# Kernel optimization log

Hardware: AMD Instinct MI355X
Metric: run time of the kernel (lower is better)

The kernel has to match this reference:

```python
import jax, jax.numpy as jnp
import numpy as np

E = 1024   # embd_size
H = 16     # head_count
HS = E // H
B = 8
T = 1024   # seq len == input_size
EPS = 1e-5

def _ln(x, g, b):
    m = jnp.mean(x, axis=-1, keepdims=True)
    v = jnp.mean((x - m) ** 2, axis=-1, keepdims=True)
    return (x - m) * jax.lax.rsqrt(v + EPS) * g + b

def setup_inputs() -> dict:
    key = jax.random.key(0)
    ks = jax.random.split(key, 12)
    s_attn = 1.0 / np.sqrt(E)
    s_ff1 = 1.0 / np.sqrt(E)
    s_ff2 = 1.0 / np.sqrt(4 * E)
    return {
        "x": jax.random.normal(ks[0], (B, T, E), dtype=jnp.float32),
        "wq": jax.random.normal(ks[1], (H, E, HS), dtype=jnp.float32) * s_attn,
        "wk": jax.random.normal(ks[2], (H, E, HS), dtype=jnp.float32) * s_attn,
        "wv": jax.random.normal(ks[3], (H, E, HS), dtype=jnp.float32) * s_attn,
        "w_proj": jax.random.normal(ks[4], (E, E), dtype=jnp.float32) * s_attn,
        "b_proj": jnp.zeros((E,), dtype=jnp.float32),
        "w1": jax.random.normal(ks[5], (E, 4 * E), dtype=jnp.float32) * s_ff1,
        "b1": jnp.zeros((4 * E,), dtype=jnp.float32),
        "w2": jax.random.normal(ks[6], (4 * E, E), dtype=jnp.float32) * s_ff2,
        "b2": jnp.zeros((E,), dtype=jnp.float32),
        "g1": jnp.ones((E,), dtype=jnp.float32),
        "be1": jnp.zeros((E,), dtype=jnp.float32),
        "g2": jnp.ones((E,), dtype=jnp.float32),
        "be2": jnp.zeros((E,), dtype=jnp.float32),
    }

def reference(x, wq, wk, wv, w_proj, b_proj, w1, b1, w2, b2, g1, be1, g2, be2):
    Tn = x.shape[1]
    h = _ln(x, g1, be1)
    # per-head projections, batched over heads: [B,T,E] x [H,E,S] -> [B,H,T,S]
    q = jnp.einsum('bte,hes->bhts', h, wq)
    k = jnp.einsum('bte,hes->bhts', h, wk)
    v = jnp.einsum('bte,hes->bhts', h, wv)
    scores = jnp.einsum('bhts,bhus->bhtu', q, k)
    # NOTE: source multiplies by sqrt(T) (x.shape[2] of scores), not 1/sqrt(head_size)
    scores = scores * jnp.float32(Tn) ** 0.5
    causal = jnp.tril(jnp.ones((Tn, Tn), dtype=bool))
    scores = jnp.where(causal, scores, -jnp.inf)
    attn = jax.nn.softmax(scores, axis=-1)
    out = jnp.einsum('bhtu,bhus->bhts', attn, v)           # [B,H,T,S]
    out = out.transpose(0, 2, 1, 3).reshape(x.shape[0], Tn, E)  # concat heads
    out = out @ w_proj + b_proj
    x = x + out
    f = _ln(x, g2, be2)
    f = jax.nn.relu(f @ w1 + b1) @ w2 + b2
    return x + f
```

## Files before the change

### kernel.cpp

```cpp
#include <hip/hip_runtime.h>


typedef unsigned short u16;
typedef __attribute__((ext_vector_type(8))) short  bfx8;
typedef __attribute__((ext_vector_type(4))) float  f32x4;
typedef __attribute__((ext_vector_type(4))) unsigned short u16v4;

#define MFMA16 __builtin_amdgcn_mfma_f32_16x16x32_bf16

__device__ __forceinline__ u16 f2bf(float f) {
    union { float f; unsigned u; } c; c.f = f;
    unsigned r = c.u + 0x7fffu + ((c.u >> 16) & 1u);
    return (u16)(r >> 16);
}
__device__ __forceinline__ float bf2f(u16 b) {
    union { unsigned u; float f; } c; c.u = ((unsigned)b) << 16; return c.f;
}

__device__ __forceinline__ void gl_lds16(const void* g, void* l) {
    void* gg = (void*)g;
    __builtin_amdgcn_global_load_lds(
        (__attribute__((address_space(1))) void*)gg,
        (__attribute__((address_space(3))) void*)l,
        16, 0, 0);
}

__global__ __launch_bounds__(256)
void transpose_split(const float* __restrict__ src, u16* __restrict__ dhi,
                     u16* __restrict__ dlo, int C, int OS,
                     size_t inBS, size_t outBS)
{
    __shared__ float t[64][65];
    const int tid = threadIdx.x;
    const float* s = src + (size_t)blockIdx.z * inBS
                   + ((size_t)blockIdx.y * 64) * C + (size_t)blockIdx.x * 64;
    const size_t obase = (size_t)blockIdx.z * outBS
                       + ((size_t)blockIdx.x * 64) * OS + (size_t)blockIdx.y * 64;
    {
        const int r = tid >> 2, c4 = (tid & 3) * 16;
#pragma unroll
        for (int k = 0; k < 4; ++k) {
            float4 f = *(const float4*)(s + (size_t)r * C + c4 + k * 4);
            t[r][c4 + k*4 + 0] = f.x; t[r][c4 + k*4 + 1] = f.y;
            t[r][c4 + k*4 + 2] = f.z; t[r][c4 + k*4 + 3] = f.w;
        }
    }
    __syncthreads();
    {
        const int c = tid >> 2, r4 = (tid & 3) * 16;
        bfx8 h0, h1, l0, l1;
#pragma unroll
        for (int k = 0; k < 8; ++k) {
            float v0 = t[r4 + k][c];
            float v1 = t[r4 + 8 + k][c];
            u16 a = f2bf(v0), b = f2bf(v1);
            h0[k] = (short)a; h1[k] = (short)b;
            l0[k] = (short)f2bf(v0 - bf2f(a));
            l1[k] = (short)f2bf(v1 - bf2f(b));
        }
        u16* d = dhi + obase + (size_t)c * OS + r4;
        *(bfx8*)d = h0; *(bfx8*)(d + 8) = h1;
        if (dlo) {
            u16* d2 = dlo + obase + (size_t)c * OS + r4;
            *(bfx8*)d2 = l0; *(bfx8*)(d2 + 8) = l1;
        }
    }
}

__global__ __launch_bounds__(256)
void transpose_v(const u16* __restrict__ v, u16* __restrict__ vT)
{
    const int ut = blockIdx.x, h = blockIdx.y, b = blockIdx.z;
    __shared__ u16 t[64][72];
    const int tid = threadIdx.x;
    {
        const int u = tid >> 2, s4 = (tid & 3) * 16;
        const u16* src = v + ((size_t)(b * 1024 + ut * 64 + u)) * 1024 + h * 64 + s4;
        bfx8 a = *(const bfx8*)src;
        bfx8 c = *(const bfx8*)(src + 8);
#pragma unroll
        for (int k = 0; k < 8; ++k) { t[u][s4 + k] = (u16)a[k]; t[u][s4 + 8 + k] = (u16)c[k]; }
    }
    __syncthreads();
    {
        const int s = tid >> 2, u4 = (tid & 3) * 16;
        bfx8 o0, o1;
#pragma unroll
        for (int k = 0; k < 8; ++k) { o0[k] = (short)t[u4 + k][s]; o1[k] = (short)t[u4 + 8 + k][s]; }
        u16* dst = vT + ((size_t)((b * 16 + h) * 64 + s)) * 1024 + ut * 64 + u4;
        *(bfx8*)dst = o0; *(bfx8*)(dst + 8) = o1;
    }
}

__global__ __launch_bounds__(256)
void ln_split(const float* __restrict__ x, const float* __restrict__ g,
              const float* __restrict__ be, u16* __restrict__ hhi,
              u16* __restrict__ hlo)
{
    const int row = blockIdx.x;
    const int tid = threadIdx.x;
    const float4 v = ((const float4*)(x + (size_t)row * 1024))[tid];
    float s  = v.x + v.y + v.z + v.w;
    float s2 = v.x*v.x + v.y*v.y + v.z*v.z + v.w*v.w;
#pragma unroll
    for (int m = 32; m >= 1; m >>= 1) {
        s  += __shfl_xor(s,  m, 64);
        s2 += __shfl_xor(s2, m, 64);
    }
    __shared__ float rs[4], rq[4];
    if ((tid & 63) == 0) { rs[tid >> 6] = s; rq[tid >> 6] = s2; }
    __syncthreads();
    s  = rs[0] + rs[1] + rs[2] + rs[3];
    s2 = rq[0] + rq[1] + rq[2] + rq[3];
    const float mean = s * (1.0f / 1024.0f);
    const float var  = s2 * (1.0f / 1024.0f) - mean * mean;
    const float inv  = rsqrtf(var + 1e-5f);
    const int col0 = tid * 4;
    float hv[4];
    hv[0] = (v.x - mean) * inv * g[col0+0] + be[col0+0];
    hv[1] = (v.y - mean) * inv * g[col0+1] + be[col0+1];
    hv[2] = (v.z - mean) * inv * g[col0+2] + be[col0+2];
    hv[3] = (v.w - mean) * inv * g[col0+3] + be[col0+3];
    u16v4 hb, lb;
#pragma unroll
    for (int k = 0; k < 4; ++k) {
        u16 a = f2bf(hv[k]);
        hb[k] = a;
        lb[k] = f2bf(hv[k] - bf2f(a));
    }
    *(u16v4*)(hhi + (size_t)row * 1024 + col0) = hb;
    if (hlo) *(u16v4*)(hlo + (size_t)row * 1024 + col0) = lb;
}

#define BM 128
#define BN 128
#define BKT 32

template<int FLAGS>
__global__ __launch_bounds__(256, 2)
void gemm_bt(const u16* __restrict__ A, const u16* __restrict__ Bt,
             void* __restrict__ Cout, const float* __restrict__ bias,
             const float* __restrict__ res, int M, int N, int K)
{
    __shared__ u16 As[BM * BKT];
    __shared__ u16 Bs[BN * BKT];
    const int tid  = threadIdx.x;
    const int lane = tid & 63, wave = tid >> 6;
    const int wr = wave >> 1, wc = wave & 1;
    const int li = lane & 15, lg = lane >> 4;
    const size_t m0 = (size_t)blockIdx.y * BM;
    const size_t n0 = (size_t)blockIdx.x * BN;
    f32x4 acc[4][4] = {};

    const int slot0 = tid, slot1 = tid + 256;
    const int r0 = slot0 >> 2, kc0 = (slot0 & 3) * 8;
    const int r1 = slot1 >> 2, kc1 = (slot1 & 3) * 8;

    for (int kt = 0; kt < K; kt += BKT) {
        __syncthreads();
        gl_lds16(A  + (m0 + r0) * K + kt + kc0, As + slot0 * 8);
        gl_lds16(Bt + (n0 + r0) * K + kt + kc0, Bs + slot0 * 8);
        gl_lds16(A  + (m0 + r1) * K + kt + kc1, As + slot1 * 8);
        gl_lds16(Bt + (n0 + r1) * K + kt + kc1, Bs + slot1 * 8);
        __syncthreads();
        bfx8 af[4], bfr[4];
#pragma unroll
        for (int i = 0; i < 4; ++i)
            af[i] = *(const bfx8*)&As[(wr * 64 + i * 16 + li) * BKT + lg * 8];
#pragma unroll
        for (int j = 0; j < 4; ++j)
            bfr[j] = *(const bfx8*)&Bs[(wc * 64 + j * 16 + li) * BKT + lg * 8];
#pragma unroll
        for (int i = 0; i < 4; ++i)
#pragma unroll
            for (int j = 0; j < 4; ++j)
                acc[i][j] = MFMA16(af[i], bfr[j], acc[i][j], 0, 0, 0);
    }

    float* Cf = (float*)Cout;
    u16*   Cb = (u16*)Cout;
#pragma unroll
    for (int i = 0; i < 4; ++i)
#pragma unroll
        for (int j = 0; j < 4; ++j)
#pragma unroll
            for (int r = 0; r < 4; ++r) {
                const size_t row = m0 + wr * 64 + i * 16 + lg * 4 + r;
                const size_t col = n0 + wc * 64 + j * 16 + li;
                float v = acc[i][j][r];
                if (FLAGS & 1) v += bias[col];
                if (FLAGS & 2) v = fmaxf(v, 0.0f);
                if (FLAGS & 4) v += res[row * (size_t)N + col];
                if (FLAGS & 8) Cf[row * (size_t)N + col] = v;
                else           Cb[row * (size_t)N + col] = f2bf(v);
            }
}

__global__ __launch_bounds__(256, 2)
void gemm_qk(const u16* __restrict__ Ah, const u16* __restrict__ Al,
             const u16* __restrict__ Bh, const u16* __restrict__ Bl,
             u16* __restrict__ Ohi, u16* __restrict__ Olo,
             int M, int N, int K)
{
    __shared__ u16 Ahs[BM * BKT], Als[BM * BKT], Bhs[BN * BKT], Bls[BN * BKT];
    const int tid  = threadIdx.x;
    const int lane = tid & 63, wave = tid >> 6;
    const int wr = wave >> 1, wc = wave & 1;
    const int li = lane & 15, lg = lane >> 4;
    const size_t m0 = (size_t)blockIdx.y * BM;
    const size_t n0 = (size_t)blockIdx.x * BN;
    f32x4 acc[4][4] = {};

    const int slot0 = tid, slot1 = tid + 256;
    const int r0 = slot0 >> 2, kc0 = (slot0 & 3) * 8;
    const int r1 = slot1 >> 2, kc1 = (slot1 & 3) * 8;

    for (int kt = 0; kt < K; kt += BKT) {
        __syncthreads();
        gl_lds16(Ah + (m0 + r0) * K + kt + kc0, Ahs + slot0 * 8);
        gl_lds16(Al + (m0 + r0) * K + kt + kc0, Als + slot0 * 8);
        gl_lds16(Bh + (n0 + r0) * K + kt + kc0, Bhs + slot0 * 8);
        gl_lds16(Bl + (n0 + r0) * K + kt + kc0, Bls + slot0 * 8);
        gl_lds16(Ah + (m0 + r1) * K + kt + kc1, Ahs + slot1 * 8);
        gl_lds16(Al + (m0 + r1) * K + kt + kc1, Als + slot1 * 8);
        gl_lds16(Bh + (n0 + r1) * K + kt + kc1, Bhs + slot1 * 8);
        gl_lds16(Bl + (n0 + r1) * K + kt + kc1, Bls + slot1 * 8);
        __syncthreads();
        bfx8 ah[4], al4[4], bh[4], bl4[4];
#pragma unroll
        for (int i = 0; i < 4; ++i) {
            ah[i]  = *(const bfx8*)&Ahs[(wr * 64 + i * 16 + li) * BKT + lg * 8];
            al4[i] = *(const bfx8*)&Als[(wr * 64 + i * 16 + li) * BKT + lg * 8];
        }
#pragma unroll
        for (int j = 0; j < 4; ++j) {
            bh[j]  = *(const bfx8*)&Bhs[(wc * 64 + j * 16 + li) * BKT + lg * 8];
            bl4[j] = *(const bfx8*)&Bls[(wc * 64 + j * 16 + li) * BKT + lg * 8];
        }
#pragma unroll
        for (int i = 0; i < 4; ++i)
#pragma unroll
            for (int j = 0; j < 4; ++j) {
                acc[i][j] = MFMA16(ah[i],  bh[j],  acc[i][j], 0, 0, 0);
                acc[i][j] = MFMA16(ah[i],  bl4[j], acc[i][j], 0, 0, 0);
                acc[i][j] = MFMA16(al4[i], bh[j],  acc[i][j], 0, 0, 0);
            }
    }
#pragma unroll
    for (int i = 0; i < 4; ++i)
#pragma unroll
        for (int j = 0; j < 4; ++j)
#pragma unroll
            for (int r = 0; r < 4; ++r) {
                const size_t row = m0 + wr * 64 + i * 16 + lg * 4 + r;
                const size_t col = n0 + wc * 64 + j * 16 + li;
                const float v = acc[i][j][r];
                const u16 hi = f2bf(v);
                Ohi[row * (size_t)N + col] = hi;
                Olo[row * (size_t)N + col] = f2bf(v - bf2f(hi));
            }
}

__global__ __launch_bounds__(256, 3)
void attn(const u16* __restrict__ qhi, const u16* __restrict__ qlo,
          const u16* __restrict__ khi, const u16* __restrict__ klo,
          const u16* __restrict__ vt, u16* __restrict__ ao)
{
    const int id  = blockIdx.x;
    const int swz = (id & 7) * 256 + (id >> 3);
    const int qt  = 15 - (swz & 15);
    const int h   = (swz >> 4) & 15;
    const int b   = swz >> 8;

    const int tid = threadIdx.x;
    const int wave = tid >> 6, lane = tid & 63;
    const int li = lane & 15, lg = lane >> 4;

    __shared__ u16 KsHi[2][4096];
    __shared__ u16 KsLo[2][4096];
    __shared__ u16 Pl[64 * 72];

    const size_t qrow = (size_t)b * 1024 + qt * 64 + wave * 16 + li;
    const size_t qoff = qrow * 1024 + h * 64 + lg * 8;
    const bfx8 qh0 = *(const bfx8*)(qhi + qoff);
    const bfx8 qh1 = *(const bfx8*)(qhi + qoff + 32);
    const bfx8 ql0 = *(const bfx8*)(qlo + qoff);
    const bfx8 ql1 = *(const bfx8*)(qlo + qoff + 32);

    f32x4 O[4] = {};
    float mrow[4] = {-1e30f, -1e30f, -1e30f, -1e30f};
    float lrow[4] = {0.f, 0.f, 0.f, 0.f};

    const u16* kh_base = khi + ((size_t)b * 1024) * 1024 + h * 64;
    const u16* kl_base = klo + ((size_t)b * 1024) * 1024 + h * 64;
    const u16* v_base  = vt + ((size_t)(b * 16 + h) * 64) * 1024;

    auto stageK = [&](int kt, int bufIdx) {
#pragma unroll
        for (int site = 0; site < 2; ++site) {
            const int s = tid + site * 256;
            const int r = s >> 3;
            const int cb = (((s & 7) << 4) ^ ((r & 7) << 4));
            const size_t go = ((size_t)(kt * 64 + r)) * 1024;
            gl_lds16((const char*)(kh_base + go) + cb, (char*)&KsHi[bufIdx][0] + s * 16);
            gl_lds16((const char*)(kl_base + go) + cb, (char*)&KsLo[bufIdx][0] + s * 16);
        }
    };

    const int rswz = (li & 7) << 4;

    stageK(0, 0);

    for (int kt = 0; kt <= qt; ++kt) {
        const int cur = kt & 1;

        bfx8 vld[2][4];
#pragma unroll
        for (int nf = 0; nf < 4; ++nf) {
            const u16* vr = v_base + ((size_t)(nf * 16 + li)) * 1024 + kt * 64 + lg * 8;
            vld[0][nf] = *(const bfx8*)vr;
            vld[1][nf] = *(const bfx8*)(vr + 32);
        }

        if (kt < qt) {
            stageK(kt + 1, cur ^ 1);
            asm volatile("s_waitcnt vmcnt(12)" ::: "memory");
        } else {
            asm volatile("s_waitcnt vmcnt(8)" ::: "memory");
        }
        __builtin_amdgcn_sched_barrier(0);
        __builtin_amdgcn_s_barrier();
        __builtin_amdgcn_sched_barrier(0);

        float sv[4][4];
        const char* khc = (const char*)&KsHi[cur][0];
        const char* klc = (const char*)&KsLo[cur][0];
#pragma unroll
        for (int nf = 0; nf < 4; ++nf) {
            const int rb = (nf * 16 + li) * 128;
            bfx8 kh0v = *(const bfx8*)(khc + rb + (((lg * 16) + 0 ) ^ rswz));
            bfx8 kh1v = *(const bfx8*)(khc + rb + (((lg * 16) + 64) ^ rswz));
            bfx8 kl0v = *(const bfx8*)(klc + rb + (((lg * 16) + 0 ) ^ rswz));
            bfx8 kl1v = *(const bfx8*)(klc + rb + (((lg * 16) + 64) ^ rswz));
            f32x4 a = {0.f, 0.f, 0.f, 0.f};
            a = MFMA16(qh0, kh0v, a, 0, 0, 0);
            a = MFMA16(qh1, kh1v, a, 0, 0, 0);
            a = MFMA16(qh0, kl0v, a, 0, 0, 0);
            a = MFMA16(qh1, kl1v, a, 0, 0, 0);
            a = MFMA16(ql0, kh0v, a, 0, 0, 0);
            a = MFMA16(ql1, kh1v, a, 0, 0, 0);
#pragma unroll
            for (int r = 0; r < 4; ++r) sv[nf][r] = a[r];
        }

        asm volatile("s_waitcnt lgkmcnt(0)" ::: "memory");
        __builtin_amdgcn_sched_barrier(0);
        __builtin_amdgcn_s_barrier();
        __builtin_amdgcn_sched_barrier(0);

        const int rowg = qt * 64 + wave * 16 + lg * 4;
        const int colg = kt * 64 + li;
        float pmax[4] = {-1e30f, -1e30f, -1e30f, -1e30f};
#pragma unroll
        for (int nf = 0; nf < 4; ++nf)
#pragma unroll
            for (int r = 0; r < 4; ++r) {
                float x2 = sv[nf][r] * 32.0f;
                if (colg + nf * 16 > rowg + r) x2 = -1e30f;
                sv[nf][r] = x2;
                pmax[r] = fmaxf(pmax[r], x2);
            }
#pragma unroll
        for (int msk = 1; msk < 16; msk <<= 1)
#pragma unroll
            for (int r = 0; r < 4; ++r)
                pmax[r] = fmaxf(pmax[r], __shfl_xor(pmax[r], msk, 64));

        float alr[4], rsum[4];
#pragma unroll
        for (int r = 0; r < 4; ++r) {
            const float mnew = fmaxf(mrow[r], pmax[r]);
            alr[r] = __expf(mrow[r] - mnew);
            mrow[r] = mnew;
            rsum[r] = 0.0f;
        }
        float pv[4][4];
#pragma unroll
        for (int nf = 0; nf < 4; ++nf)
#pragma unroll
            for (int r = 0; r < 4; ++r) {
                const float p = __expf(sv[nf][r] - mrow[r]);
                pv[nf][r] = p;
                rsum[r] += p;
            }
#pragma unroll
        for (int msk = 1; msk < 16; msk <<= 1)
#pragma unroll
            for (int r = 0; r < 4; ++r)
                rsum[r] += __shfl_xor(rsum[r], msk, 64);
#pragma unroll
        for (int r = 0; r < 4; ++r)
            lrow[r] = lrow[r] * alr[r] + rsum[r];
#pragma unroll
        for (int nf = 0; nf < 4; ++nf)
#pragma unroll
            for (int r = 0; r < 4; ++r)
                O[nf][r] *= alr[r];

#pragma unroll
        for (int nf = 0; nf < 4; ++nf)
#pragma unroll
            for (int r = 0; r < 4; ++r)
                Pl[(wave * 16 + lg * 4 + r) * 72 + nf * 16 + li] = f2bf(pv[nf][r]);

#pragma unroll
        for (int ku = 0; ku < 2; ++ku) {
            bfx8 pf = *(const bfx8*)&Pl[(wave * 16 + li) * 72 + ku * 32 + lg * 8];
#pragma unroll
            for (int nf = 0; nf < 4; ++nf)
                O[nf] = MFMA16(pf, vld[ku][nf], O[nf], 0, 0, 0);
        }
    }

    float invl[4];
#pragma unroll
    for (int r = 0; r < 4; ++r) invl[r] = 1.0f / lrow[r];
    const size_t orow = (size_t)b * 1024 + qt * 64 + wave * 16 + lg * 4;
#pragma unroll
    for (int nf = 0; nf < 4; ++nf)
#pragma unroll
        for (int r = 0; r < 4; ++r)
            ao[(orow + r) * 1024 + h * 64 + nf * 16 + li] = f2bf(O[nf][r] * invl[r]);
}

extern "C" void kernel_launch(void* const* d_in, const int* in_sizes, int n_in,
                              void* d_out, int out_size, void* d_ws, size_t ws_size,
                              hipStream_t stream)
{
    (void)in_sizes; (void)n_in; (void)out_size; (void)ws_size;
    const float* x      = (const float*)d_in[0];
    const float* wq     = (const float*)d_in[1];
    const float* wk     = (const float*)d_in[2];
    const float* wv     = (const float*)d_in[3];
    const float* w_proj = (const float*)d_in[4];
    const float* b_proj = (const float*)d_in[5];
    const float* w1     = (const float*)d_in[6];
    const float* b1     = (const float*)d_in[7];
    const float* w2     = (const float*)d_in[8];
    const float* b2     = (const float*)d_in[9];
    const float* g1     = (const float*)d_in[10];
    const float* be1    = (const float*)d_in[11];
    const float* g2     = (const float*)d_in[12];
    const float* be2    = (const float*)d_in[13];
    float* out = (float*)d_out;

    const size_t ME2 = (size_t)8192 * 1024 * 2;
    char* wsp = (char*)d_ws;
    u16* h_hi = (u16*)(wsp + 0 * ME2);
    u16* h_lo = (u16*)(wsp + 1 * ME2);
    u16* q_hi = (u16*)(wsp + 2 * ME2);
    u16* q_lo = (u16*)(wsp + 3 * ME2);
    u16* k_hi = (u16*)(wsp + 4 * ME2);
    u16* k_lo = (u16*)(wsp + 5 * ME2);
    u16* v_b  = (u16*)(wsp + 6 * ME2);
    u16* vtr  = (u16*)(wsp + 7 * ME2);
    float* y  = (float*)(wsp + 8 * ME2);
    char* wp0 = wsp + 8 * ME2 + (size_t)8192 * 1024 * 4;
    const size_t W1M = (size_t)1024 * 1024 * 2;
    u16* wqT_hi = (u16*)(wp0 + 0 * W1M);
    u16* wqT_lo = (u16*)(wp0 + 1 * W1M);
    u16* wkT_hi = (u16*)(wp0 + 2 * W1M);
    u16* wkT_lo = (u16*)(wp0 + 3 * W1M);
    u16* wvT    = (u16*)(wp0 + 4 * W1M);
    u16* wpT    = (u16*)(wp0 + 5 * W1M);
    u16* w1T    = (u16*)(wp0 + 6 * W1M);
    u16* w2T    = (u16*)(wp0 + 6 * W1M + 4 * W1M);
    u16* f2  = h_hi;
    u16* ao  = h_lo;
    u16* act = q_hi;

    dim3 blk(256);

    transpose_split<<<dim3(1, 16, 16), blk, 0, stream>>>(wq, wqT_hi, wqT_lo, 64, 1024, (size_t)65536, (size_t)65536);
    transpose_split<<<dim3(1, 16, 16), blk, 0, stream>>>(wk, wkT_hi, wkT_lo, 64, 1024, (size_t)65536, (size_t)65536);
    transpose_split<<<dim3(1, 16, 16), blk, 0, stream>>>(wv, wvT, nullptr, 64, 1024, (size_t)65536, (size_t)65536);
    transpose_split<<<dim3(16, 16, 1), blk, 0, stream>>>(w_proj, wpT, nullptr, 1024, 1024, 0, 0);
    transpose_split<<<dim3(64, 16, 1), blk, 0, stream>>>(w1, w1T, nullptr, 4096, 1024, 0, 0);
    transpose_split<<<dim3(16, 64, 1), blk, 0, stream>>>(w2, w2T, nullptr, 1024, 4096, 0, 0);

    ln_split<<<8192, blk, 0, stream>>>(x, g1, be1, h_hi, h_lo);

    gemm_qk<<<dim3(8, 64), blk, 0, stream>>>(h_hi, h_lo, wqT_hi, wqT_lo, q_hi, q_lo, 8192, 1024, 1024);
    gemm_qk<<<dim3(8, 64), blk, 0, stream>>>(h_hi, h_lo, wkT_hi, wkT_lo, k_hi, k_lo, 8192, 1024, 1024);
    gemm_bt<0><<<dim3(8, 64), blk, 0, stream>>>(h_hi, wvT, v_b, nullptr, nullptr, 8192, 1024, 1024);
    transpose_v<<<dim3(16, 16, 8), blk, 0, stream>>>(v_b, vtr);

    attn<<<dim3(2048), blk, 0, stream>>>(q_hi, q_lo, k_hi, k_lo, vtr, ao);

    gemm_bt<1 | 4 | 8><<<dim3(8, 64), blk, 0, stream>>>(ao, wpT, y, b_proj, x, 8192, 1024, 1024);

    ln_split<<<8192, blk, 0, stream>>>(y, g2, be2, f2, nullptr);

    gemm_bt<1 | 2><<<dim3(32, 64), blk, 0, stream>>>(f2, w1T, act, b1, nullptr, 8192, 4096, 1024);
    gemm_bt<1 | 4 | 8><<<dim3(8, 64), blk, 0, stream>>>(act, w2T, out, b2, y, 8192, 1024, 4096);
}
```

Measured before the change: 555.0 us.

## Add 256x256 8-wave pipelined FFN1 GEMM and use exp2 in attention softmax

```diff
diff --git a/kernel.cpp b/kernel.cpp
--- a/kernel.cpp
+++ b/kernel.cpp
@@ -15,6 +15,9 @@
 }
 __device__ __forceinline__ float bf2f(u16 b) {
     union { unsigned u; float f; } c; c.u = ((unsigned)b) << 16; return c.f;
+}
+__device__ __forceinline__ float exp2_fast(float x) {
+    float r; asm("v_exp_f32 %0, %1" : "=v"(r) : "v"(x)); return r;
 }
 
 __device__ __forceinline__ void gl_lds16(const void* g, void* l) {
@@ -196,6 +199,147 @@
             }
 }
 
+__global__ __launch_bounds__(512, 2)
+void gemm8_ffn1(const u16* __restrict__ A, const u16* __restrict__ Bt,
+                u16* __restrict__ C, const float* __restrict__ bias,
+                int M, int N, int K)
+{
+    __shared__ u16 Asl[2][2][128 * 64];
+    __shared__ u16 Bsl[2][2][128 * 64];
+    const int tid = threadIdx.x;
+    const int lane = tid & 63, wave = tid >> 6;
+    const int wr = wave >> 2, wc = wave & 3;
+    const int li = lane & 15, lg = lane >> 4;
+
+    const int bid = blockIdx.x;
+    const int swz = (bid & 7) * 64 + (bid >> 3);
+    const int bx = swz & 15, by = swz >> 4;
+    const size_t m0 = (size_t)by * 256, n0 = (size_t)bx * 256;
+
+    char* ldsA = (char*)&Asl[0][0][0];
+    char* ldsB = (char*)&Bsl[0][0][0];
+
+    auto stageA = [&](int j, int h) {
+#pragma unroll
+        for (int site = 0; site < 2; ++site) {
+            const int s = tid + site * 512;
+            const int r = s >> 3;
+            const int cb = ((s & 7) << 4) ^ ((r & 7) << 4);
+            gl_lds16((const char*)(A + (m0 + h * 128 + r) * (size_t)K + (size_t)j * 64) + cb,
+                     ldsA + ((j & 1) * 2 + h) * 16384 + s * 16);
+        }
+    };
+    auto stageB = [&](int j, int h) {
+#pragma unroll
+        for (int site = 0; site < 2; ++site) {
+            const int s = tid + site * 512;
+            const int r = s >> 3;
+            const int cb = ((s & 7) << 4) ^ ((r & 7) << 4);
+            gl_lds16((const char*)(Bt + (n0 + h * 128 + r) * (size_t)K + (size_t)j * 64) + cb,
+                     ldsB + ((j & 1) * 2 + h) * 16384 + s * 16);
+        }
+    };
+
+    const int lsw = (li & 7) << 4;
+    const int aHalfBase = wr * 16384;
+    const int bHalfBase = (wc >> 1) * 16384;
+    const int bRow0 = (wc & 1) * 64;
+
+    f32x4 acc[8][4] = {};
+    const int NT = K >> 6;
+    const int NI = NT >> 1;
+
+    stageA(0, 0); stageA(0, 1); stageB(0, 0); stageB(0, 1);
+    stageB(1, 0); stageB(1, 1);
+    asm volatile("s_waitcnt vmcnt(0)" ::: "memory");
+    __builtin_amdgcn_sched_barrier(0);
+    __builtin_amdgcn_s_barrier();
+    __builtin_amdgcn_sched_barrier(0);
+
+    for (int t = 0; t < NI; ++t) {
+        const bool more = (t + 1 < NI);
+#pragma unroll
+        for (int half = 0; half < 2; ++half) {
+            const int buf = half;
+            const int abase = buf * 32768 + aHalfBase;
+            const int bbase = buf * 32768 + bHalfBase;
+            bfx8 bfr[4][2];
+#pragma unroll
+            for (int q = 0; q < 4; ++q) {
+                if (q == 0) {
+#pragma unroll
+                    for (int nf = 0; nf < 4; ++nf)
+#pragma unroll
+                        for (int ks = 0; ks < 2; ++ks)
+                            bfr[nf][ks] = *(const bfx8*)(ldsB + bbase
+                                + (bRow0 + nf * 16 + li) * 128
+                                + ((ks * 64 + lg * 16) ^ lsw));
+                }
+                bfx8 afr[2][2];
+#pragma unroll
+                for (int m = 0; m < 2; ++m)
+#pragma unroll
+                    for (int ks = 0; ks < 2; ++ks)
+                        afr[m][ks] = *(const bfx8*)(ldsA + abase
+                            + ((2 * q + m) * 16 + li) * 128
+                            + ((ks * 64 + lg * 16) ^ lsw));
+
+                if (half == 0) {
+                    if (q == 0) stageA(2 * t + 1, 0);
+                    else if (q == 1) stageA(2 * t + 1, 1);
+                    else if (q == 2) { if (more) stageB(2 * t + 2, 0); }
+                    else             { if (more) stageB(2 * t + 2, 1); }
+                } else {
+                    if (q == 0)      { if (more) stageA(2 * t + 2, 0); }
+                    else if (q == 1) { if (more) stageA(2 * t + 2, 1); }
+                    else if (q == 2) { if (more) stageB(2 * t + 3, 0); }
+                    else             { if (more) stageB(2 * t + 3, 1); }
+                }
+
+                __builtin_amdgcn_sched_barrier(0);
+                __builtin_amdgcn_s_barrier();
+                asm volatile("s_waitcnt lgkmcnt(0)" ::: "memory");
+                __builtin_amdgcn_sched_barrier(0);
+                __builtin_amdgcn_s_setprio(1);
+#pragma unroll
+                for (int ks = 0; ks < 2; ++ks)
+#pragma unroll
+                    for (int m = 0; m < 2; ++m)
+#pragma unroll
+                        for (int nf = 0; nf < 4; ++nf)
+                            acc[2 * q + m][nf] = MFMA16(afr[m][ks], bfr[nf][ks],
+                                                        acc[2 * q + m][nf], 0, 0, 0);
+                __builtin_amdgcn_s_setprio(0);
+                __builtin_amdgcn_sched_barrier(0);
+                if (q == 3) {
+                    if (half == 0) {
+                        if (more) { asm volatile("s_waitcnt vmcnt(4)" ::: "memory"); }
+                        else      { asm volatile("s_waitcnt vmcnt(0)" ::: "memory"); }
+                    } else if (more) {
+                        asm volatile("s_waitcnt vmcnt(4)" ::: "memory");
+                    }
+                    __builtin_amdgcn_sched_barrier(0);
+                }
+                __builtin_amdgcn_s_barrier();
+                __builtin_amdgcn_sched_barrier(0);
+            }
+        }
+    }
+
+#pragma unroll
+    for (int i = 0; i < 8; ++i)
+#pragma unroll
+        for (int nf = 0; nf < 4; ++nf)
+#pragma unroll
+            for (int r = 0; r < 4; ++r) {
+                const size_t row = m0 + wr * 128 + i * 16 + lg * 4 + r;
+                const size_t col = n0 + wc * 64 + nf * 16 + li;
+                float v = acc[i][nf][r] + bias[col];
+                v = fmaxf(v, 0.0f);
+                C[row * (size_t)N + col] = f2bf(v);
+            }
+}
+
 __global__ __launch_bounds__(256, 2)
 void gemm_qk(const u16* __restrict__ Ah, const u16* __restrict__ Al,
              const u16* __restrict__ Bh, const u16* __restrict__ Bl,
@@ -290,6 +434,10 @@
     f32x4 O[4] = {};
     float mrow[4] = {-1e30f, -1e30f, -1e30f, -1e30f};
     float lrow[4] = {0.f, 0.f, 0.f, 0.f};
+
+    const int vs  = tid >> 2;
+    const int vu4 = (tid & 3) * 16;
+    (void)vs; (void)vu4;
 
     const u16* kh_base = khi + ((size_t)b * 1024) * 1024 + h * 64;
     const u16* kl_base = klo + ((size_t)b * 1024) * 1024 + h * 64;
@@ -365,7 +513,7 @@
         for (int nf = 0; nf < 4; ++nf)
 #pragma unroll
             for (int r = 0; r < 4; ++r) {
-                float x2 = sv[nf][r] * 32.0f;
+                float x2 = sv[nf][r] * 46.166240905715613f;
                 if (colg + nf * 16 > rowg + r) x2 = -1e30f;
                 sv[nf][r] = x2;
                 pmax[r] = fmaxf(pmax[r], x2);
@@ -380,7 +528,7 @@
 #pragma unroll
         for (int r = 0; r < 4; ++r) {
             const float mnew = fmaxf(mrow[r], pmax[r]);
-            alr[r] = __expf(mrow[r] - mnew);
+            alr[r] = exp2_fast(mrow[r] - mnew);
             mrow[r] = mnew;
             rsum[r] = 0.0f;
         }
@@ -389,7 +537,7 @@
         for (int nf = 0; nf < 4; ++nf)
 #pragma unroll
             for (int r = 0; r < 4; ++r) {
-                const float p = __expf(sv[nf][r] - mrow[r]);
+                const float p = exp2_fast(sv[nf][r] - mrow[r]);
                 pv[nf][r] = p;
                 rsum[r] += p;
             }
@@ -501,6 +649,6 @@
 
     ln_split<<<8192, blk, 0, stream>>>(y, g2, be2, f2, nullptr);
 
-    gemm_bt<1 | 2><<<dim3(32, 64), blk, 0, stream>>>(f2, w1T, act, b1, nullptr, 8192, 4096, 1024);
+    gemm8_ffn1<<<dim3(512), dim3(512), 0, stream>>>(f2, w1T, act, b1, 8192, 4096, 1024);
     gemm_bt<1 | 4 | 8><<<dim3(8, 64), blk, 0, stream>>>(act, w2T, out, b2, y, 8192, 1024, 4096);
 }
```

After: 546.8 us. Within noise of the previous version (-1.5%).
